# Kernel optimization log

Hardware: AMD Instinct MI355X
Metric: run time of the kernel (lower is better)

The kernel has to match this reference:

```python
import jax, jax.numpy as jnp
import numpy as np

B, C, T, P, K = 8, 512, 8192, 512, 30


def _linear_params(key, fan_in, fan_out):
    kw, kb = jax.random.split(key)
    s = 1.0 / np.sqrt(fan_in)
    W = jax.random.uniform(kw, (fan_out, fan_in), jnp.float32, -s, s)
    b = jax.random.uniform(kb, (fan_out,), jnp.float32, -s, s)
    return W, b


def setup_inputs() -> dict:
    key = jax.random.key(0)
    ks = jax.random.split(key, 7)
    x = jax.random.normal(ks[0], (B, C, T), jnp.float32)
    # valid proposals: 0 <= start < end <= T, length in [1, 256]
    starts = jax.random.randint(ks[1], (B, P), 0, T - 256)
    lens = jax.random.randint(ks[2], (B, P), 1, 257)
    ends = jnp.minimum(starts + lens, T)
    proposal_boxes = jnp.stack([starts, ends], axis=-1).astype(jnp.int64)
    W6, b6 = _linear_params(ks[3], C, 1024)
    W7, b7 = _linear_params(ks[4], 1024, 512)
    Wc, bc = _linear_params(ks[5], 512, K)
    Wd, bd = _linear_params(ks[6], 512, K)
    return dict(x=x, proposal_boxes=proposal_boxes, W6=W6, b6=b6, W7=W7, b7=b7,
                Wc=Wc, bc=bc, Wd=Wd, bd=bd)


def reference(x, proposal_boxes, W6, b6, W7, b7, Wc, bc, Wd, bd):
    Bx, Cx, Tx = x.shape
    # segment mean via prefix sums: mean(x[b,:,s:e]) = (cs[e]-cs[s])/(e-s)
    cs = jnp.concatenate(
        [jnp.zeros((Bx, Cx, 1), x.dtype), jnp.cumsum(x, axis=2)], axis=2)  # [B,C,T+1]
    starts = proposal_boxes[..., 0]  # [B,P]
    ends = proposal_boxes[..., 1]    # [B,P]
    gs = jnp.take_along_axis(cs, starts[:, None, :], axis=2)  # [B,C,P]
    ge = jnp.take_along_axis(cs, ends[:, None, :], axis=2)    # [B,C,P]
    seg_len = (ends - starts).astype(x.dtype)[:, None, :]      # [B,1,P]
    pooled = (ge - gs) / seg_len                               # [B,C,P]
    feats = jnp.transpose(pooled, (0, 2, 1))                   # [B,P,C]

    h6 = jax.nn.relu(feats @ W6.T + b6)   # [B,P,1024]
    h7 = jax.nn.relu(h6 @ W7.T + b7)      # [B,P,512]
    class_logits = h7 @ Wc.T + bc         # [B,P,K]
    det_logits = h7 @ Wd.T + bd           # [B,P,K]
    class_prob = jax.nn.softmax(class_logits, axis=2)
    det_prob = jax.nn.softmax(det_logits, axis=1)
    joint_prob = class_prob * det_prob
    video_prob = joint_prob.sum(axis=1)   # [B,K]
    return (video_prob, joint_prob, class_logits, det_logits, h7)
```

## Files before the change

kernel.cpp:

```cpp
#include <hip/hip_runtime.h>
#include <hip/hip_bf16.h>

#define B_ 8
#define C_ 512
#define T_ 8192
#define P_ 512
#define K_ 30

typedef __attribute__((ext_vector_type(8))) short bf16x8;
typedef __attribute__((ext_vector_type(4))) float f32x4;

__device__ __forceinline__ unsigned short f2bf(float f) {
    union { float f; unsigned u; } v; v.f = f;
    unsigned r = v.u + 0x7fff + ((v.u >> 16) & 1);
    return (unsigned short)(r >> 16);
}

#define SCAN_PAD(i) ((i) + ((i) >> 5))

__global__ __launch_bounds__(256) void f32_to_bf16_kernel(
    const float* __restrict__ in, unsigned short* __restrict__ out, int n)
{
    int i = (blockIdx.x * 256 + threadIdx.x) * 4;
    if (i < n) {
        float4 v = *(const float4*)(in + i);
        ushort4 o;
        o.x = f2bf(v.x); o.y = f2bf(v.y); o.z = f2bf(v.z); o.w = f2bf(v.w);
        *(ushort4*)(out + i) = o;
    }
}

__global__ __launch_bounds__(256) void pool_scan_kernel(
    const float* __restrict__ x, const int* __restrict__ boxes,
    unsigned short* __restrict__ featsT)
{
    __shared__ float cs[8448];
    __shared__ float wtot[4];

    int bc  = blockIdx.x;
    int b   = bc >> 9;
    int tid = threadIdx.x;
    int lane = tid & 63, wave = tid >> 6;

    const float* row = x + (size_t)bc * T_;
    for (int i = tid; i < T_; i += 256)
        cs[SCAN_PAD(i)] = row[i];
    __syncthreads();

    int base = tid * 32;
    float run = 0.f;
    #pragma unroll
    for (int i = 0; i < 32; ++i) {
        run += cs[SCAN_PAD(base + i)];
        cs[SCAN_PAD(base + i)] = run;
    }

    float v = run;
    #pragma unroll
    for (int off = 1; off < 64; off <<= 1) {
        float n = __shfl_up(v, off);
        if (lane >= off) v += n;
    }
    if (lane == 63) wtot[wave] = v;
    __syncthreads();
    float waveoff = 0.f;
    #pragma unroll
    for (int wv = 0; wv < 4; ++wv)
        if (wv < wave) waveoff += wtot[wv];
    float excl = (v - run) + waveoff;

    #pragma unroll
    for (int i = 0; i < 32; ++i)
        cs[SCAN_PAD(base + i)] += excl;
    __syncthreads();

    const int* bx = boxes + b * P_ * 2;
    for (int p = tid; p < P_; p += 256) {
        int s = bx[2 * p], e = bx[2 * p + 1];
        float hi = cs[SCAN_PAD(e - 1)];
        float lo = (s > 0) ? cs[SCAN_PAD(s - 1)] : 0.f;
        featsT[(size_t)bc * P_ + p] = f2bf((hi - lo) / (float)(e - s));
    }
}

__global__ __launch_bounds__(256) void transpose_kernel(
    const unsigned short* __restrict__ featsT, unsigned short* __restrict__ feats)
{
    __shared__ unsigned short tile[64][68];
    int c0 = blockIdx.x * 64;
    int p0 = blockIdx.y * 64;
    int b  = blockIdx.z;
    int tid = threadIdx.x;
    int tx = tid & 15;
    int ty = tid >> 4;

    #pragma unroll
    for (int rr = 0; rr < 4; ++rr) {
        int c = rr * 16 + ty;
        ushort4 v = *(const ushort4*)(featsT +
            ((size_t)(b * C_ + c0 + c) * P_ + p0 + tx * 4));
        tile[c][tx * 4 + 0] = v.x; tile[c][tx * 4 + 1] = v.y;
        tile[c][tx * 4 + 2] = v.z; tile[c][tx * 4 + 3] = v.w;
    }
    __syncthreads();
    #pragma unroll
    for (int rr = 0; rr < 4; ++rr) {
        int p = rr * 16 + ty;
        ushort4 o;
        o.x = tile[tx * 4 + 0][p]; o.y = tile[tx * 4 + 1][p];
        o.z = tile[tx * 4 + 2][p]; o.w = tile[tx * 4 + 3][p];
        *(ushort4*)(feats + ((size_t)(b * P_ + p0 + p) * C_ + c0 + tx * 4)) = o;
    }
}

template<int K, int RELU, int OUT_BF16>
__global__ __launch_bounds__(256) void gemm_mfma(
    const unsigned short* __restrict__ A, const unsigned short* __restrict__ Bw,
    const float* __restrict__ bias, void* __restrict__ out, int N)
{
    int tid  = threadIdx.x;
    int lane = tid & 63;
    int w    = tid >> 6;
    int lr   = lane & 15;
    int lk   = (lane >> 4) * 8;

    int m_base = blockIdx.y * 128 + (w & 1) * 64;
    int n_base = blockIdx.x * 128 + (w >> 1) * 64;

    const unsigned short* Ap = A + (size_t)(m_base + lr) * K + lk;
    const unsigned short* Bp = Bw + (size_t)(n_base + lr) * K + lk;

    f32x4 acc[4][4] = {};

    for (int k0 = 0; k0 < K; k0 += 32) {
        bf16x8 a[4], b[4];
        #pragma unroll
        for (int mi = 0; mi < 4; ++mi)
            a[mi] = *(const bf16x8*)(Ap + (size_t)mi * 16 * K + k0);
        #pragma unroll
        for (int ni = 0; ni < 4; ++ni)
            b[ni] = *(const bf16x8*)(Bp + (size_t)ni * 16 * K + k0);
        #pragma unroll
        for (int mi = 0; mi < 4; ++mi)
            #pragma unroll
            for (int ni = 0; ni < 4; ++ni)
                acc[mi][ni] = __builtin_amdgcn_mfma_f32_16x16x32_bf16(
                    a[mi], b[ni], acc[mi][ni], 0, 0, 0);
    }

    int rbase0 = (lane >> 4) * 4;
    #pragma unroll
    for (int ni = 0; ni < 4; ++ni) {
        int col = n_base + ni * 16 + lr;
        float bv = bias[col];
        #pragma unroll
        for (int mi = 0; mi < 4; ++mi) {
            int rbase = m_base + mi * 16 + rbase0;
            #pragma unroll
            for (int r = 0; r < 4; ++r) {
                float v = acc[mi][ni][r] + bv;
                if (RELU) v = fmaxf(v, 0.f);
                if (OUT_BF16)
                    ((unsigned short*)out)[(size_t)(rbase + r) * N + col] = f2bf(v);
                else
                    ((float*)out)[(size_t)(rbase + r) * N + col] = v;
            }
        }
    }
}

__global__ __launch_bounds__(64) void heads_kernel(
    const float* __restrict__ h7,
    const float* __restrict__ Wc, const float* __restrict__ bc,
    const float* __restrict__ Wd, const float* __restrict__ bd,
    float* __restrict__ class_logits, float* __restrict__ det_logits,
    float* __restrict__ class_prob)
{
    int bp = blockIdx.x;
    int lane = threadIdx.x;
    const float* hrow = h7 + (size_t)bp * 512;

    float h[8];
    #pragma unroll
    for (int j = 0; j < 8; ++j) h[j] = hrow[lane + 64 * j];

    __shared__ float sm[64];

    for (int k = 0; k < K_; ++k) {
        const float* w = Wc + (size_t)k * 512;
        float acc = 0.f;
        #pragma unroll
        for (int j = 0; j < 8; ++j) acc += h[j] * w[lane + 64 * j];
        #pragma unroll
        for (int off = 32; off; off >>= 1) acc += __shfl_xor(acc, off);
        if (lane == 0) sm[k] = acc + bc[k];
    }
    for (int k = 0; k < K_; ++k) {
        const float* w = Wd + (size_t)k * 512;
        float acc = 0.f;
        #pragma unroll
        for (int j = 0; j < 8; ++j) acc += h[j] * w[lane + 64 * j];
        #pragma unroll
        for (int off = 32; off; off >>= 1) acc += __shfl_xor(acc, off);
        if (lane == 0) sm[K_ + k] = acc + bd[k];
    }
    __syncthreads();

    float lc = (lane < K_) ? sm[lane] : -3.4e38f;
    if (lane < K_) {
        class_logits[(size_t)bp * K_ + lane] = lc;
        det_logits[(size_t)bp * K_ + lane]   = sm[K_ + lane];
    }
    float mx = lc;
    #pragma unroll
    for (int off = 32; off; off >>= 1) mx = fmaxf(mx, __shfl_xor(mx, off));
    float ex = (lane < K_) ? __expf(lc - mx) : 0.f;
    float sum = ex;
    #pragma unroll
    for (int off = 32; off; off >>= 1) sum += __shfl_xor(sum, off);
    if (lane < K_) class_prob[(size_t)bp * K_ + lane] = ex / sum;
}

__global__ __launch_bounds__(256) void det_softmax_kernel(
    const float* __restrict__ det_logits, const float* __restrict__ class_prob,
    float* __restrict__ joint, float* __restrict__ video)
{
    int k = blockIdx.x;
    int b = blockIdx.y;
    int tid = threadIdx.x;
    size_t base = (size_t)b * P_ * K_ + k;

    float v0 = det_logits[base + (size_t)tid * K_];
    float v1 = det_logits[base + (size_t)(tid + 256) * K_];

    __shared__ float red[256];
    red[tid] = fmaxf(v0, v1);
    __syncthreads();
    for (int off = 128; off; off >>= 1) {
        if (tid < off) red[tid] = fmaxf(red[tid], red[tid + off]);
        __syncthreads();
    }
    float mx = red[0];
    __syncthreads();

    float e0 = __expf(v0 - mx), e1 = __expf(v1 - mx);
    red[tid] = e0 + e1;
    __syncthreads();
    for (int off = 128; off; off >>= 1) {
        if (tid < off) red[tid] += red[tid + off];
        __syncthreads();
    }
    float inv = 1.0f / red[0];
    __syncthreads();

    float j0 = class_prob[base + (size_t)tid * K_] * e0 * inv;
    float j1 = class_prob[base + (size_t)(tid + 256) * K_] * e1 * inv;
    joint[base + (size_t)tid * K_] = j0;
    joint[base + (size_t)(tid + 256) * K_] = j1;

    red[tid] = j0 + j1;
    __syncthreads();
    for (int off = 128; off; off >>= 1) {
        if (tid < off) red[tid] += red[tid + off];
        __syncthreads();
    }
    if (tid == 0) video[(size_t)b * K_ + k] = red[0];
}

extern "C" void kernel_launch(void* const* d_in, const int* in_sizes, int n_in,
                              void* d_out, int out_size, void* d_ws, size_t ws_size,
                              hipStream_t stream)
{
    const float* x     = (const float*)d_in[0];
    const int*   boxes = (const int*)d_in[1];
    const float* W6 = (const float*)d_in[2];
    const float* b6 = (const float*)d_in[3];
    const float* W7 = (const float*)d_in[4];
    const float* b7 = (const float*)d_in[5];
    const float* Wc = (const float*)d_in[6];
    const float* bc = (const float*)d_in[7];
    const float* Wd = (const float*)d_in[8];
    const float* bd = (const float*)d_in[9];

    float* out          = (float*)d_out;
    float* video        = out;
    float* joint        = out + 240;
    float* class_logits = out + 123120;
    float* det_logits   = out + 246000;
    float* h7           = out + 368880;

    unsigned short* feats  = (unsigned short*)h7;
    unsigned short* featsT = feats + (size_t)4096 * 512;
    float* class_prob      = joint;

    unsigned short* h6  = (unsigned short*)d_ws;
    unsigned short* w6b = h6 + (size_t)4096 * 1024;
    unsigned short* w7b = w6b + (size_t)1024 * 512;

    const int M = B_ * P_;

    f32_to_bf16_kernel<<<512, 256, 0, stream>>>(W6, w6b, 1024 * 512);
    f32_to_bf16_kernel<<<512, 256, 0, stream>>>(W7, w7b, 512 * 1024);

    pool_scan_kernel<<<B_ * C_, 256, 0, stream>>>(x, boxes, featsT);

    transpose_kernel<<<dim3(C_ / 64, P_ / 64, B_), 256, 0, stream>>>(featsT, feats);

    gemm_mfma<512, 1, 1><<<dim3(1024 / 128, M / 128), 256, 0, stream>>>(
        feats, w6b, b6, (void*)h6, 1024);

    gemm_mfma<1024, 1, 0><<<dim3(512 / 128, M / 128), 256, 0, stream>>>(
        h6, w7b, b7, (void*)h7, 512);

    heads_kernel<<<M, 64, 0, stream>>>(
        h7, Wc, bc, Wd, bd, class_logits, det_logits, class_prob);

    det_softmax_kernel<<<dim3(K_, B_), 256, 0, stream>>>(
        det_logits, class_prob, joint, video);
}
```

Before: 319.0 us.

## Fuse weight conversion into pooling kernel and run heads as bf16 MFMA GEMM

Merges the two weight-conversion launches into the pooling kernel as extra blocks, which also pack Wc/Wd into a padded bf16 matrix. The pooling scan now loads each thread's 32 elements straight into registers with float4 loads instead of staging them through shared memory first. The second GEMM also writes a bf16 copy of h7, and a new 16-block MFMA kernel computes both heads and the class softmax, replacing the one-wave-per-row scalar heads kernel. This cuts launches and scalar FMA work, but the heads now use bf16 inputs (lower precision) and run on only 16 blocks.

After: 293.3 us. -8.1%, faster.

```diff
diff --git a/kernel.cpp b/kernel.cpp
--- a/kernel.cpp
+++ b/kernel.cpp
@@ -18,64 +18,88 @@
 
 #define SCAN_PAD(i) ((i) + ((i) >> 5))
 
-__global__ __launch_bounds__(256) void f32_to_bf16_kernel(
-    const float* __restrict__ in, unsigned short* __restrict__ out, int n)
-{
-    int i = (blockIdx.x * 256 + threadIdx.x) * 4;
-    if (i < n) {
-        float4 v = *(const float4*)(in + i);
-        ushort4 o;
-        o.x = f2bf(v.x); o.y = f2bf(v.y); o.z = f2bf(v.z); o.w = f2bf(v.w);
-        *(ushort4*)(out + i) = o;
-    }
-}
-
-__global__ __launch_bounds__(256) void pool_scan_kernel(
+__global__ __launch_bounds__(256) void prep_pool_kernel(
     const float* __restrict__ x, const int* __restrict__ boxes,
-    unsigned short* __restrict__ featsT)
+    unsigned short* __restrict__ featsT,
+    const float* __restrict__ W6, unsigned short* __restrict__ w6b,
+    const float* __restrict__ W7, unsigned short* __restrict__ w7b,
+    const float* __restrict__ Wc, const float* __restrict__ bcv,
+    const float* __restrict__ Wd, const float* __restrict__ bdv,
+    unsigned short* __restrict__ wcd, float* __restrict__ bcd)
 {
     __shared__ float cs[8448];
     __shared__ float wtot[4];
 
-    int bc  = blockIdx.x;
-    int b   = bc >> 9;
+    int bid = blockIdx.x;
     int tid = threadIdx.x;
+
+    if (bid >= 4096) {
+        int j = bid - 4096;
+        if (j < 512) {
+            int i = j * 1024 + tid * 4;
+            float4 v = *(const float4*)(W6 + i);
+            ushort4 o; o.x = f2bf(v.x); o.y = f2bf(v.y);
+            o.z = f2bf(v.z); o.w = f2bf(v.w);
+            *(ushort4*)(w6b + i) = o;
+        } else if (j < 1024) {
+            int i = (j - 512) * 1024 + tid * 4;
+            float4 v = *(const float4*)(W7 + i);
+            ushort4 o; o.x = f2bf(v.x); o.y = f2bf(v.y);
+            o.z = f2bf(v.z); o.w = f2bf(v.w);
+            *(ushort4*)(w7b + i) = o;
+        } else {
+            int r = j - 1024;
+            const float* src = nullptr;
+            float bias = 0.f;
+            if (r < 30)                 { src = Wc + (size_t)r * 512;        bias = bcv[r]; }
+            else if (r >= 32 && r < 62) { src = Wd + (size_t)(r - 32) * 512; bias = bdv[r - 32]; }
+            #pragma unroll
+            for (int q = 0; q < 2; ++q) {
+                int c = tid + q * 256;
+                wcd[(size_t)r * 512 + c] = src ? f2bf(src[c]) : (unsigned short)0;
+            }
+            if (tid == 0) bcd[r] = bias;
+        }
+        return;
+    }
+
+    int bc = bid;
+    int b  = bc >> 9;
     int lane = tid & 63, wave = tid >> 6;
-
     const float* row = x + (size_t)bc * T_;
-    for (int i = tid; i < T_; i += 256)
-        cs[SCAN_PAD(i)] = row[i];
-    __syncthreads();
 
     int base = tid * 32;
+    float v[32];
+    #pragma unroll
+    for (int q = 0; q < 8; ++q)
+        *(float4*)&v[q * 4] = *(const float4*)(row + base + q * 4);
     float run = 0.f;
     #pragma unroll
-    for (int i = 0; i < 32; ++i) {
-        run += cs[SCAN_PAD(base + i)];
-        cs[SCAN_PAD(base + i)] = run;
-    }
-
-    float v = run;
+    for (int i = 0; i < 32; ++i) { run += v[i]; v[i] = run; }
+
+    float sc = run;
     #pragma unroll
     for (int off = 1; off < 64; off <<= 1) {
-        float n = __shfl_up(v, off);
-        if (lane >= off) v += n;
-    }
-    if (lane == 63) wtot[wave] = v;
-    __syncthreads();
-    float waveoff = 0.f;
+        float n = __shfl_up(sc, off);
+        if (lane >= off) sc += n;
+    }
+    if (lane == 63) wtot[wave] = sc;
+    __syncthreads();
+    float woff = 0.f;
     #pragma unroll
     for (int wv = 0; wv < 4; ++wv)
-        if (wv < wave) waveoff += wtot[wv];
-    float excl = (v - run) + waveoff;
+        if (wv < wave) woff += wtot[wv];
+    float excl = (sc - run) + woff;
 
     #pragma unroll
     for (int i = 0; i < 32; ++i)
-        cs[SCAN_PAD(base + i)] += excl;
+        cs[SCAN_PAD(base + i)] = v[i] + excl;
     __syncthreads();
 
     const int* bx = boxes + b * P_ * 2;
-    for (int p = tid; p < P_; p += 256) {
+    #pragma unroll
+    for (int q = 0; q < 2; ++q) {
+        int p = tid + q * 256;
         int s = bx[2 * p], e = bx[2 * p + 1];
         float hi = cs[SCAN_PAD(e - 1)];
         float lo = (s > 0) ? cs[SCAN_PAD(s - 1)] : 0.f;
@@ -113,10 +137,11 @@
     }
 }
 
-template<int K, int RELU, int OUT_BF16>
+template<int K, int RELU, int MODE>
 __global__ __launch_bounds__(256) void gemm_mfma(
     const unsigned short* __restrict__ A, const unsigned short* __restrict__ Bw,
-    const float* __restrict__ bias, void* __restrict__ out, int N)
+    const float* __restrict__ bias, void* __restrict__ out,
+    unsigned short* __restrict__ out2, int N)
 {
     int tid  = threadIdx.x;
     int lane = tid & 63;
@@ -160,65 +185,80 @@
             for (int r = 0; r < 4; ++r) {
                 float v = acc[mi][ni][r] + bv;
                 if (RELU) v = fmaxf(v, 0.f);
-                if (OUT_BF16)
-                    ((unsigned short*)out)[(size_t)(rbase + r) * N + col] = f2bf(v);
-                else
-                    ((float*)out)[(size_t)(rbase + r) * N + col] = v;
+                size_t idx = (size_t)(rbase + r) * N + col;
+                if (MODE == 1) ((unsigned short*)out)[idx] = f2bf(v);
+                else           ((float*)out)[idx] = v;
+                if (MODE == 2) out2[idx] = f2bf(v);
             }
         }
     }
 }
 
-__global__ __launch_bounds__(64) void heads_kernel(
-    const float* __restrict__ h7,
-    const float* __restrict__ Wc, const float* __restrict__ bc,
-    const float* __restrict__ Wd, const float* __restrict__ bd,
+__global__ __launch_bounds__(256) void heads_gemm_kernel(
+    const unsigned short* __restrict__ h7b,
+    const unsigned short* __restrict__ wcd, const float* __restrict__ bcd,
     float* __restrict__ class_logits, float* __restrict__ det_logits,
     float* __restrict__ class_prob)
 {
-    int bp = blockIdx.x;
-    int lane = threadIdx.x;
-    const float* hrow = h7 + (size_t)bp * 512;
-
-    float h[8];
-    #pragma unroll
-    for (int j = 0; j < 8; ++j) h[j] = hrow[lane + 64 * j];
-
-    __shared__ float sm[64];
-
-    for (int k = 0; k < K_; ++k) {
-        const float* w = Wc + (size_t)k * 512;
-        float acc = 0.f;
-        #pragma unroll
-        for (int j = 0; j < 8; ++j) acc += h[j] * w[lane + 64 * j];
-        #pragma unroll
-        for (int off = 32; off; off >>= 1) acc += __shfl_xor(acc, off);
-        if (lane == 0) sm[k] = acc + bc[k];
-    }
-    for (int k = 0; k < K_; ++k) {
-        const float* w = Wd + (size_t)k * 512;
-        float acc = 0.f;
-        #pragma unroll
-        for (int j = 0; j < 8; ++j) acc += h[j] * w[lane + 64 * j];
-        #pragma unroll
-        for (int off = 32; off; off >>= 1) acc += __shfl_xor(acc, off);
-        if (lane == 0) sm[K_ + k] = acc + bd[k];
-    }
-    __syncthreads();
-
-    float lc = (lane < K_) ? sm[lane] : -3.4e38f;
-    if (lane < K_) {
-        class_logits[(size_t)bp * K_ + lane] = lc;
-        det_logits[(size_t)bp * K_ + lane]   = sm[K_ + lane];
-    }
-    float mx = lc;
-    #pragma unroll
-    for (int off = 32; off; off >>= 1) mx = fmaxf(mx, __shfl_xor(mx, off));
-    float ex = (lane < K_) ? __expf(lc - mx) : 0.f;
-    float sum = ex;
-    #pragma unroll
-    for (int off = 32; off; off >>= 1) sum += __shfl_xor(sum, off);
-    if (lane < K_) class_prob[(size_t)bp * K_ + lane] = ex / sum;
+    int tid  = threadIdx.x;
+    int lane = tid & 63;
+    int w    = tid >> 6;
+    int lr   = lane & 15;
+    int lk   = (lane >> 4) * 8;
+
+    int m_base = blockIdx.x * 256 + w * 64;
+
+    const unsigned short* Ap = h7b + (size_t)(m_base + lr) * 512 + lk;
+    const unsigned short* Bp = wcd + (size_t)lr * 512 + lk;
+
+    f32x4 acc[4][4] = {};
+
+    for (int k0 = 0; k0 < 512; k0 += 32) {
+        bf16x8 a[4], b[4];
+        #pragma unroll
+        for (int mi = 0; mi < 4; ++mi)
+            a[mi] = *(const bf16x8*)(Ap + (size_t)mi * 16 * 512 + k0);
+        #pragma unroll
+        for (int ni = 0; ni < 4; ++ni)
+            b[ni] = *(const bf16x8*)(Bp + (size_t)ni * 16 * 512 + k0);
+        #pragma unroll
+        for (int mi = 0; mi < 4; ++mi)
+            #pragma unroll
+            for (int ni = 0; ni < 4; ++ni)
+                acc[mi][ni] = __builtin_amdgcn_mfma_f32_16x16x32_bf16(
+                    a[mi], b[ni], acc[mi][ni], 0, 0, 0);
+    }
+
+    float b0 = bcd[lr], b1 = bcd[16 + lr], b2 = bcd[32 + lr], b3 = bcd[48 + lr];
+    int rgrp = (lane >> 4) * 4;
+
+    #pragma unroll
+    for (int mi = 0; mi < 4; ++mi) {
+        #pragma unroll
+        for (int r = 0; r < 4; ++r) {
+            int row = m_base + mi * 16 + rgrp + r;
+            float c0 = acc[mi][0][r] + b0;
+            float c1 = (lr < 14) ? (acc[mi][1][r] + b1) : -3.4e38f;
+            float mx = fmaxf(c0, c1);
+            #pragma unroll
+            for (int m = 1; m < 16; m <<= 1) mx = fmaxf(mx, __shfl_xor(mx, m));
+            float e0 = __expf(c0 - mx);
+            float e1 = (lr < 14) ? __expf(c1 - mx) : 0.f;
+            float s = e0 + e1;
+            #pragma unroll
+            for (int m = 1; m < 16; m <<= 1) s += __shfl_xor(s, m);
+            float inv = 1.0f / s;
+
+            class_logits[(size_t)row * K_ + lr] = c0;
+            class_prob[(size_t)row * K_ + lr]   = e0 * inv;
+            det_logits[(size_t)row * K_ + lr]   = acc[mi][2][r] + b2;
+            if (lr < 14) {
+                class_logits[(size_t)row * K_ + 16 + lr] = c1;
+                class_prob[(size_t)row * K_ + 16 + lr]   = e1 * inv;
+                det_logits[(size_t)row * K_ + 16 + lr]   = acc[mi][3][r] + b3;
+            }
+        }
+    }
 }
 
 __global__ __launch_bounds__(256) void det_softmax_kernel(
@@ -289,31 +329,32 @@
     float* det_logits   = out + 246000;
     float* h7           = out + 368880;
 
-    unsigned short* feats  = (unsigned short*)h7;
-    unsigned short* featsT = feats + (size_t)4096 * 512;
-    float* class_prob      = joint;
-
-    unsigned short* h6  = (unsigned short*)d_ws;
-    unsigned short* w6b = h6 + (size_t)4096 * 1024;
-    unsigned short* w7b = w6b + (size_t)1024 * 512;
+    unsigned short* wsu   = (unsigned short*)d_ws;
+    unsigned short* h6    = wsu;
+    unsigned short* w6b   = h6 + (size_t)4096 * 1024;
+    unsigned short* w7b   = w6b + (size_t)1024 * 512;
+    unsigned short* wcd   = w7b + (size_t)512 * 1024;
+    unsigned short* h7b   = wcd + (size_t)64 * 512;
+    unsigned short* feats = h7b + (size_t)4096 * 512;
+    unsigned short* featsT= feats + (size_t)4096 * 512;
+    float* bcd            = (float*)(featsT + (size_t)4096 * 512);
+    float* class_prob     = bcd + 64;
 
     const int M = B_ * P_;
 
-    f32_to_bf16_kernel<<<512, 256, 0, stream>>>(W6, w6b, 1024 * 512);
-    f32_to_bf16_kernel<<<512, 256, 0, stream>>>(W7, w7b, 512 * 1024);
-
-    pool_scan_kernel<<<B_ * C_, 256, 0, stream>>>(x, boxes, featsT);
+    prep_pool_kernel<<<5184, 256, 0, stream>>>(
+        x, boxes, featsT, W6, w6b, W7, w7b, Wc, bc, Wd, bd, wcd, bcd);
 
     transpose_kernel<<<dim3(C_ / 64, P_ / 64, B_), 256, 0, stream>>>(featsT, feats);
 
     gemm_mfma<512, 1, 1><<<dim3(1024 / 128, M / 128), 256, 0, stream>>>(
-        feats, w6b, b6, (void*)h6, 1024);
-
-    gemm_mfma<1024, 1, 0><<<dim3(512 / 128, M / 128), 256, 0, stream>>>(
-        h6, w7b, b7, (void*)h7, 512);
-
-    heads_kernel<<<M, 64, 0, stream>>>(
-        h7, Wc, bc, Wd, bd, class_logits, det_logits, class_prob);
+        feats, w6b, b6, (void*)h6, nullptr, 1024);
+
+    gemm_mfma<1024, 1, 2><<<dim3(512 / 128, M / 128), 256, 0, stream>>>(
+        h6, w7b, b7, (void*)h7, h7b, 512);
+
+    heads_gemm_kernel<<<16, 256, 0, stream>>>(
+        h7b, wcd, bcd, class_logits, det_logits, class_prob);
 
     det_softmax_kernel<<<dim3(K_, B_), 256, 0, stream>>>(
         det_logits, class_prob, joint, video);
```
